# Performance work log

Measured on AMD Instinct MI355X. Metric: run time of the kernel, lower is better.

## Reference

```python
import jax, jax.numpy as jnp
import numpy as np
from jax import lax

# dims
B, N, D, H, K, NS = 16, 4096, 64, 128, 32, 1024  # clouds, pts/cloud, feat, hidden, max neighbors, fps samples
R = 0.2  # radius


def _fps(pos, n_s):
    """Farthest point sampling on one cloud. pos: [N,3] -> idx [n_s] int32."""
    n = pos.shape[0]

    def step(carry, _):
        dist, last = carry
        d = jnp.sum((pos - pos[last]) ** 2, axis=-1)
        dist = jnp.minimum(dist, d)
        nxt = jnp.argmax(dist).astype(jnp.int32)
        return (dist, nxt), last

    init = (jnp.full((n,), 1e10, pos.dtype), jnp.int32(0))
    _, idx = lax.scan(step, init, None, length=n_s)
    return idx


def setup_inputs() -> dict:
    key = jax.random.key(0)
    ks = jax.random.split(key, 6)
    s1 = 1.0 / np.sqrt(D + 1)
    s2 = 1.0 / np.sqrt(H)
    s3 = 1.0 / np.sqrt(D + H)
    return {
        "x": jax.random.normal(ks[0], (B, N, D), jnp.float32),
        "pos": jax.random.uniform(ks[1], (B, N, 3), jnp.float32),
        "W1": jax.random.normal(ks[2], (D + 1, H), jnp.float32) * s1,
        "b1": jnp.zeros((H,), jnp.float32),
        "W2": jax.random.normal(ks[3], (H, 3), jnp.float32) * s2,
        "b2": jnp.zeros((3,), jnp.float32),
        "W3": jax.random.normal(ks[4], (D + H, H), jnp.float32) * s3,
        "b3": jnp.zeros((H,), jnp.float32),
    }


def reference(x, pos, W1, b1, W2, b2, W3, b3):
    # 1) FPS downsample per cloud -> centers
    idx = jax.vmap(lambda p: _fps(p, NS))(pos)                    # [B,NS]
    pos_s = jax.vmap(lambda p, i: p[i])(pos, idx)                 # [B,NS,3]

    # 2) radius neighbor search: nearest-K within R (<= max_num_neighbors=32)
    d2 = jnp.sum((pos_s[:, :, None, :] - pos[:, None, :, :]) ** 2, axis=-1)  # [B,NS,N]
    masked = jnp.where(d2 <= R * R, d2, jnp.inf)
    neg, nbr = lax.top_k(-masked, K)                              # nearest K
    valid = (-neg) <= R * R                                       # [B,NS,K]

    # 3) gather neighbor features/positions
    x_j = jax.vmap(lambda a, i: a[i])(x, nbr)                     # [B,NS,K,D]
    pos_j = jax.vmap(lambda a, i: a[i])(pos, nbr)                 # [B,NS,K,3]
    diff = pos_j - pos_s[:, :, None, :]                           # pos_j - pos_i
    d2sel = jnp.sum(diff ** 2, axis=-1)
    dist = jnp.where(d2sel > 0, jnp.sqrt(jnp.where(d2sel > 0, d2sel, 1.0)), 0.0)

    # 4) message MLPs
    feat = jnp.concatenate([x_j, dist[..., None]], axis=-1)       # [B,NS,K,D+1]
    emb = jax.nn.relu(feat @ W1 + b1)                             # nn_msg_x
    pw = emb @ W2 + b2                                            # nn_msg_pos
    pmsg = diff * pw

    # 5) masked aggregate: sum for x, mean for pos
    m = valid[..., None].astype(emb.dtype)
    aggr_x = jnp.sum(emb * m, axis=2)                             # [B,NS,H]
    cnt = jnp.maximum(jnp.sum(m, axis=2), 1.0)                    # [B,NS,1]
    aggr_pos = jnp.sum(pmsg * m, axis=2) / cnt                    # [B,NS,3]

    # 6) update
    x_d = jax.vmap(lambda a, i: a[i])(x, idx)                     # [B,NS,D]
    out_x = jax.nn.relu(jnp.concatenate([x_d, aggr_x], axis=-1) @ W3 + b3)
    out_pos = pos_s + aggr_pos
    return out_x, out_pos, idx
```

## Files before the change

### kernel.cpp

```cpp
#include <hip/hip_runtime.h>
#include <math.h>

#define B_ 16
#define N_ 4096
#define D_ 64
#define H_ 128
#define K_ 32
#define NS_ 1024
#define R2_ 0.04f
#define CAP_ 1024

typedef short short8 __attribute__((ext_vector_type(8)));
typedef float f32x4 __attribute__((ext_vector_type(4)));
typedef unsigned short ushort_t;

static __device__ __forceinline__ short f2bf(float f) {
    unsigned u = __float_as_uint(f);
    unsigned r = (u + 0x7FFFu + ((u >> 16) & 1u)) >> 16;
    return (short)r;
}

template<int CTRL, int RM>
static __device__ __forceinline__ unsigned dppmov(unsigned v) {
    return (unsigned)__builtin_amdgcn_update_dpp((int)v, (int)v, CTRL, RM, 0xF, false);
}

#define DPP_FMAX_STEP(CTRL, RM)                                           \
    {                                                                     \
        float n = __uint_as_float(dppmov<CTRL, RM>(__float_as_uint(wm))); \
        wm = fmaxf(wm, n);                                                \
    }

#define DPP_UMIN_STEP(CTRL, RM)                                           \
    {                                                                     \
        unsigned n = dppmov<CTRL, RM>(cand);                              \
        cand = n < cand ? n : cand;                                       \
    }

#define DPP_UMIN_STEP_V(var, CTRL, RM)                                    \
    {                                                                     \
        unsigned n = dppmov<CTRL, RM>(var);                               \
        var = n < var ? n : var;                                          \
    }

__global__ __launch_bounds__(256) void cvt_kernel(
    const float* __restrict__ x, ushort_t* __restrict__ xb)
{
    const size_t i = ((size_t)blockIdx.x * 256 + threadIdx.x) * 8;
    float4 a = *(const float4*)(x + i);
    float4 c = *(const float4*)(x + i + 4);
    short8 o;
    o[0] = f2bf(a.x); o[1] = f2bf(a.y); o[2] = f2bf(a.z); o[3] = f2bf(a.w);
    o[4] = f2bf(c.x); o[5] = f2bf(c.y); o[6] = f2bf(c.z); o[7] = f2bf(c.w);
    *(short8*)(xb + i) = o;
}

__global__ __launch_bounds__(256, 1) void fps_kernel(
    const float* __restrict__ pos, int* __restrict__ idx_i,
    float* __restrict__ idx_f, float* __restrict__ pos_s)
{
    __shared__ float4 lpos4[N_];
    __shared__ float4 sres[NS_];
    __shared__ unsigned long long skey[2][4];
    __shared__ float4 scoord[2][4];
    const int b = blockIdx.x;
    const int t = threadIdx.x;
    const int wv = t >> 6;
    const int lane = t & 63;
    const float* posb = pos + (size_t)b * N_ * 3;
    for (int p = t; p < N_; p += 256)
        lpos4[p] = make_float4(posb[3 * p + 0], posb[3 * p + 1], posb[3 * p + 2], 0.f);
    __syncthreads();

    float px[16], py[16], pz[16], dist[16];
#pragma unroll
    for (int j = 0; j < 16; ++j) {
        float4 v = lpos4[t + 256 * j];
        px[j] = v.x; py[j] = v.y; pz[j] = v.z;
        dist[j] = 1e10f;
    }
    unsigned curidx = 0;
    float4 c0 = lpos4[0];
    float ccx = c0.x, ccy = c0.y, ccz = c0.z;

    for (int ns = 0; ns < NS_; ++ns) {
        if (t == 0)
            sres[ns] = make_float4(ccx, ccy, ccz, __uint_as_float(curidx));
        float bv = -1.f; int bj = 0;
#pragma unroll
        for (int j = 0; j < 16; ++j) {
            float dx = __fsub_rn(px[j], ccx);
            float dy = __fsub_rn(py[j], ccy);
            float dz = __fsub_rn(pz[j], ccz);
            float d2 = __fadd_rn(__fadd_rn(__fmul_rn(dx, dx), __fmul_rn(dy, dy)), __fmul_rn(dz, dz));
            float dn = fminf(dist[j], d2);
            dist[j] = dn;
            bool g = dn > bv;
            bv = g ? dn : bv;
            bj = g ? j : bj;
        }
        float wm = bv;
        DPP_FMAX_STEP(0x111, 0xF)
        DPP_FMAX_STEP(0x112, 0xF)
        DPP_FMAX_STEP(0x114, 0xF)
        DPP_FMAX_STEP(0x118, 0xF)
        DPP_FMAX_STEP(0x142, 0xA)
        DPP_FMAX_STEP(0x143, 0xC)
        const float wavemax = __uint_as_float(
            (unsigned)__builtin_amdgcn_readlane((int)__float_as_uint(wm), 63));
        const unsigned pidx = (unsigned)t + ((unsigned)bj << 8);
        const unsigned long long mask = __ballot(bv == wavemax);
        unsigned widx;
        if (__popcll(mask) == 1) {
            const int wl = __ffsll((long long)mask) - 1;
            widx = (unsigned)__builtin_amdgcn_readlane((int)pidx, wl);
        } else {
            unsigned cand = (bv == wavemax) ? pidx : 0xFFFFFFFFu;
            DPP_UMIN_STEP(0x111, 0xF)
            DPP_UMIN_STEP(0x112, 0xF)
            DPP_UMIN_STEP(0x114, 0xF)
            DPP_UMIN_STEP(0x118, 0xF)
            DPP_UMIN_STEP(0x142, 0xA)
            DPP_UMIN_STEP(0x143, 0xC)
            widx = (unsigned)__builtin_amdgcn_readlane((int)cand, 63);
        }
        float4 wc = lpos4[widx];
        if (lane == 0) {
            skey[ns & 1][wv] = (((unsigned long long)__float_as_uint(wavemax)) << 32)
                             | (unsigned long long)(0xFFFFFFFFu - widx);
            scoord[ns & 1][wv] = wc;
        }
        __syncthreads();
        {
            unsigned sid = (unsigned)(lane & 3);
            unsigned long long skv = skey[ns & 1][sid];
            float4 scv = scoord[ns & 1][sid];
            unsigned kh2 = (unsigned)(skv >> 32), kl2 = (unsigned)skv;
#define SLOT_STEP(CTRL)                                                        \
            {                                                                  \
                unsigned nh = dppmov<CTRL, 0xF>(kh2);                          \
                unsigned nl = dppmov<CTRL, 0xF>(kl2);                          \
                unsigned nsid = dppmov<CTRL, 0xF>(sid);                        \
                unsigned long long nk = (((unsigned long long)nh) << 32) | nl; \
                unsigned long long ok = (((unsigned long long)kh2) << 32) | kl2;\
                if (nk > ok) { kh2 = nh; kl2 = nl; sid = nsid; }               \
            }
            SLOT_STEP(0x101)
            SLOT_STEP(0x102)
#undef SLOT_STEP
            const int slotwin = __builtin_amdgcn_readfirstlane((int)sid);
            curidx = 0xFFFFFFFFu - (unsigned)__builtin_amdgcn_readfirstlane((int)kl2);
            ccx = __uint_as_float((unsigned)__builtin_amdgcn_readlane(
                      (int)__float_as_uint(scv.x), slotwin));
            ccy = __uint_as_float((unsigned)__builtin_amdgcn_readlane(
                      (int)__float_as_uint(scv.y), slotwin));
            ccz = __uint_as_float((unsigned)__builtin_amdgcn_readlane(
                      (int)__float_as_uint(scv.z), slotwin));
        }
    }
    __syncthreads();
    for (int i = t; i < NS_; i += 256) {
        float4 r = sres[i];
        unsigned id = __float_as_uint(r.w);
        idx_i[b * NS_ + i] = (int)id;
        idx_f[b * NS_ + i] = (float)id;
        pos_s[(b * NS_ + i) * 3 + 0] = r.x;
        pos_s[(b * NS_ + i) * 3 + 1] = r.y;
        pos_s[(b * NS_ + i) * 3 + 2] = r.z;
    }
}

__global__ __launch_bounds__(256) void nbr_kernel(
    const float* __restrict__ pos, const float* __restrict__ pos_s,
    int* __restrict__ nbr, float* __restrict__ cntv)
{
    __shared__ unsigned long long ck[4][CAP_];
    const int w = threadIdx.x >> 6;
    const int lane = threadIdx.x & 63;
    const int s = blockIdx.x * 4 + w;
    const int b = s >> 10;
    const float cx = pos_s[s * 3 + 0], cy = pos_s[s * 3 + 1], cz = pos_s[s * 3 + 2];
    const float* posb = pos + (size_t)b * N_ * 3;
    int m = 0;
    for (int base = 0; base < N_; base += 64) {
        int p = base + lane;
        float dx = __fsub_rn(posb[3 * p + 0], cx);
        float dy = __fsub_rn(posb[3 * p + 1], cy);
        float dz = __fsub_rn(posb[3 * p + 2], cz);
        float d2 = __fadd_rn(__fadd_rn(__fmul_rn(dx, dx), __fmul_rn(dy, dy)), __fmul_rn(dz, dz));
        bool in = (d2 <= R2_);
        unsigned long long msk = __ballot(in);
        int before = __popcll(msk & ((1ull << lane) - 1ull));
        int slot = m + before;
        if (in && slot < CAP_)
            ck[w][slot] = ((unsigned long long)__float_as_uint(d2) << 32) | (unsigned)p;
        m += __popcll(msk);
    }
    if (m > CAP_) m = CAP_;
    __asm__ volatile("s_waitcnt lgkmcnt(0)" ::: "memory");
    int kcnt = m < K_ ? m : K_;
    if (m <= 256) {
        unsigned long long kr[4];
#pragma unroll
        for (int r = 0; r < 4; ++r) {
            int q = r * 64 + lane;
            unsigned long long v = ck[w][q & (CAP_ - 1)];
            kr[r] = (q < m) ? v : ~0ull;
        }
        unsigned chosen = 0;
        for (int k = 0; k < kcnt; ++k) {
            unsigned long long localk = ~0ull; int br = -1;
#pragma unroll
            for (int r = 0; r < 4; ++r) {
                bool ok = (!((chosen >> r) & 1u)) && (kr[r] < localk);
                localk = ok ? kr[r] : localk;
                br = ok ? r : br;
            }
            const unsigned mybits = (unsigned)(localk >> 32);
            const unsigned myidx = (unsigned)localk;
            unsigned wb = mybits;
            DPP_UMIN_STEP_V(wb, 0x111, 0xF)
            DPP_UMIN_STEP_V(wb, 0x112, 0xF)
            DPP_UMIN_STEP_V(wb, 0x114, 0xF)
            DPP_UMIN_STEP_V(wb, 0x118, 0xF)
            DPP_UMIN_STEP_V(wb, 0x142, 0xA)
            DPP_UMIN_STEP_V(wb, 0x143, 0xC)
            const unsigned minbits = (unsigned)__builtin_amdgcn_readlane((int)wb, 63);
            const unsigned long long wmask = __ballot(mybits == minbits);
            unsigned widx;
            if (__popcll(wmask) == 1) {
                const int wl = __ffsll((long long)wmask) - 1;
                widx = (unsigned)__builtin_amdgcn_readlane((int)myidx, wl);
            } else {
                unsigned cand = (mybits == minbits) ? myidx : 0xFFFFFFFFu;
                DPP_UMIN_STEP(0x111, 0xF)
                DPP_UMIN_STEP(0x112, 0xF)
                DPP_UMIN_STEP(0x114, 0xF)
                DPP_UMIN_STEP(0x118, 0xF)
                DPP_UMIN_STEP(0x142, 0xA)
                DPP_UMIN_STEP(0x143, 0xC)
                widx = (unsigned)__builtin_amdgcn_readlane((int)cand, 63);
            }
            if (mybits == minbits && myidx == widx) chosen |= 1u << br;
            if (lane == 0) nbr[s * K_ + k] = (int)widx;
        }
    } else {
        unsigned chosen = 0;
        for (int k = 0; k < kcnt; ++k) {
            unsigned long long localk = ~0ull; int bslot = -1;
            for (int r = 0; r * 64 + lane < m; ++r) {
                if (chosen & (1u << r)) continue;
                int q = r * 64 + lane;
                unsigned long long key = ck[w][q];
                if (key < localk) { localk = key; bslot = q; }
            }
            unsigned kh = (unsigned)(localk >> 32), kl = (unsigned)localk;
#define DPP_MIN_STEP2(CTRL, RM)                                           \
            {                                                             \
                unsigned nh = dppmov<CTRL, RM>(kh);                       \
                unsigned nl = dppmov<CTRL, RM>(kl);                       \
                unsigned long long nk = (((unsigned long long)nh) << 32) | nl; \
                unsigned long long ok = (((unsigned long long)kh) << 32) | kl; \
                if (nk < ok) { kh = nh; kl = nl; }                        \
            }
            DPP_MIN_STEP2(0x111, 0xF)
            DPP_MIN_STEP2(0x112, 0xF)
            DPP_MIN_STEP2(0x114, 0xF)
            DPP_MIN_STEP2(0x118, 0xF)
            DPP_MIN_STEP2(0x142, 0xA)
            DPP_MIN_STEP2(0x143, 0xC)
#undef DPP_MIN_STEP2
            unsigned mh = (unsigned)__builtin_amdgcn_readlane((int)kh, 63);
            unsigned ml = (unsigned)__builtin_amdgcn_readlane((int)kl, 63);
            unsigned long long bk = (((unsigned long long)mh) << 32) | ml;
            if (localk == bk && bslot >= 0) chosen |= 1u << (bslot >> 6);
            if (lane == 0) nbr[s * K_ + k] = (int)(bk & 0xFFFFFFFFull);
        }
    }
    if (lane == 0) {
        for (int k = kcnt; k < K_; ++k) nbr[s * K_ + k] = -1;
        cntv[s] = (float)kcnt;
    }
}

__global__ __launch_bounds__(256) void msg_kernel(
    const ushort_t* __restrict__ xb, const float* __restrict__ pos,
    const float* __restrict__ W1, const float* __restrict__ b1,
    const float* __restrict__ W2, const float* __restrict__ b2,
    const float* __restrict__ pos_s, const int* __restrict__ nbr,
    const float* __restrict__ cntv, float* __restrict__ aggr_x,
    float* __restrict__ out_pos)
{
    __shared__ __align__(16) char smem[4 * 5120];
    const int t = threadIdx.x;
    const int wv = t >> 6, lane = t & 63;
    const int quad = lane >> 4, cl = lane & 15;
    char* wb = smem + wv * 5120;

    short8 bfrag[8][2];
    float b1v[8], w1dv[8], w2v0[8], w2v1[8], w2v2[8];
#pragma unroll
    for (int Nt = 0; Nt < 8; ++Nt) {
        const int h = Nt * 16 + cl;
#pragma unroll
        for (int ks = 0; ks < 2; ++ks) {
            short8 f;
#pragma unroll
            for (int jj = 0; jj < 8; ++jj)
                f[jj] = f2bf(W1[(ks * 32 + quad * 8 + jj) * H_ + h]);
            bfrag[Nt][ks] = f;
        }
        b1v[Nt] = b1[h];
        w1dv[Nt] = W1[64 * H_ + h];
        w2v0[Nt] = W2[h * 3 + 0];
        w2v1[Nt] = W2[h * 3 + 1];
        w2v2[Nt] = W2[h * 3 + 2];
    }
    const float b20 = b2[0], b21 = b2[1], b22 = b2[2];

    const int kkg = lane >> 1, half = lane & 1;
    for (int i = 0; i < 4; ++i) {
        const int s = blockIdx.x * 16 + wv * 4 + i;
        const int b = s >> 10;
        const int n = nbr[s * K_ + kkg];
        {
            char* frow = wb + kkg * 144 + half * 64;
            if (n >= 0) {
                const short8* xr = (const short8*)(xb + ((size_t)b * N_ + n) * D_) + half * 4;
#pragma unroll
                for (int q = 0; q < 4; ++q) *(short8*)(frow + q * 16) = xr[q];
            } else {
                short8 z = {0, 0, 0, 0, 0, 0, 0, 0};
#pragma unroll
                for (int q = 0; q < 4; ++q) *(short8*)(frow + q * 16) = z;
            }
            if (half == 0) {
                float dxm = 0.f, dym = 0.f, dzm = 0.f, de = -1.f;
                if (n >= 0) {
                    const float* pj = pos + ((size_t)b * N_ + n) * 3;
                    float dx = pj[0] - pos_s[s * 3 + 0];
                    float dy = pj[1] - pos_s[s * 3 + 1];
                    float dz = pj[2] - pos_s[s * 3 + 2];
                    float d2 = dx * dx + dy * dy + dz * dz;
                    de = d2 > 0.f ? sqrtf(d2) : 0.f;
                    dxm = dx; dym = dy; dzm = dz;
                }
                f32x4 sv = {dxm, dym, dzm, de};
                *(f32x4*)(wb + 4608 + kkg * 16) = sv;
            }
        }
        float agp[8] = {0, 0, 0, 0, 0, 0, 0, 0};
        float gp0[8] = {0, 0, 0, 0, 0, 0, 0, 0};
        float gp1[8] = {0, 0, 0, 0, 0, 0, 0, 0};
        float gp2[8] = {0, 0, 0, 0, 0, 0, 0, 0};
#pragma unroll
        for (int Mt = 0; Mt < 2; ++Mt) {
            short8 a0 = *(short8*)(wb + (Mt * 16 + cl) * 144 + quad * 16);
            short8 a1 = *(short8*)(wb + (Mt * 16 + cl) * 144 + 64 + quad * 16);
            f32x4 acc[8];
#pragma unroll
            for (int Nt = 0; Nt < 8; ++Nt) {
                f32x4 z = {0.f, 0.f, 0.f, 0.f};
                z = __builtin_amdgcn_mfma_f32_16x16x32_bf16(a0, bfrag[Nt][0], z, 0, 0, 0);
                z = __builtin_amdgcn_mfma_f32_16x16x32_bf16(a1, bfrag[Nt][1], z, 0, 0, 0);
                acc[Nt] = z;
            }
            f32x4 sd[4];
#pragma unroll
            for (int r = 0; r < 4; ++r)
                sd[r] = *(f32x4*)(wb + 4608 + (Mt * 16 + quad * 4 + r) * 16);
#pragma unroll
            for (int Nt = 0; Nt < 8; ++Nt) {
#pragma unroll
                for (int r = 0; r < 4; ++r) {
                    float dr = sd[r][3];
                    float wgt = dr >= 0.f ? 1.f : 0.f;
                    float dd = dr >= 0.f ? dr : 0.f;
                    float e = fmaf(dd, w1dv[Nt], acc[Nt][r]) + b1v[Nt];
                    e = e > 0.f ? e : 0.f;
                    agp[Nt] = fmaf(wgt, e, agp[Nt]);
                    gp0[Nt] = fmaf(sd[r][0], e, gp0[Nt]);
                    gp1[Nt] = fmaf(sd[r][1], e, gp1[Nt]);
                    gp2[Nt] = fmaf(sd[r][2], e, gp2[Nt]);
                }
            }
        }
#pragma unroll
        for (int Nt = 0; Nt < 8; ++Nt) {
            float v = agp[Nt]; v += __shfl_xor(v, 16); v += __shfl_xor(v, 32);
            aggr_x[(size_t)s * H_ + Nt * 16 + cl] = v;
            float g0 = gp0[Nt]; g0 += __shfl_xor(g0, 16); g0 += __shfl_xor(g0, 32); gp0[Nt] = g0;
            float g1 = gp1[Nt]; g1 += __shfl_xor(g1, 16); g1 += __shfl_xor(g1, 32); gp1[Nt] = g1;
            float g2 = gp2[Nt]; g2 += __shfl_xor(g2, 16); g2 += __shfl_xor(g2, 32); gp2[Nt] = g2;
        }
        float pr0 = 0.f, pr1 = 0.f, pr2 = 0.f;
#pragma unroll
        for (int Nt = 0; Nt < 8; ++Nt) {
            pr0 = fmaf(w2v0[Nt], gp0[Nt], pr0);
            pr1 = fmaf(w2v1[Nt], gp1[Nt], pr1);
            pr2 = fmaf(w2v2[Nt], gp2[Nt], pr2);
        }
#pragma unroll
        for (int off = 1; off < 16; off <<= 1) {
            pr0 += __shfl_xor(pr0, off);
            pr1 += __shfl_xor(pr1, off);
            pr2 += __shfl_xor(pr2, off);
        }
        f32x4 dsv = *(f32x4*)(wb + 4608 + (lane & 31) * 16);
        float q0 = dsv[0], q1 = dsv[1], q2 = dsv[2];
#pragma unroll
        for (int off = 1; off < 32; off <<= 1) {
            q0 += __shfl_xor(q0, off);
            q1 += __shfl_xor(q1, off);
            q2 += __shfl_xor(q2, off);
        }
        float cnt = cntv[s]; if (cnt < 1.f) cnt = 1.f;
        if (lane < 3) {
            float pr = lane == 0 ? pr0 : (lane == 1 ? pr1 : pr2);
            float qq = lane == 0 ? q0 : (lane == 1 ? q1 : q2);
            float bb = lane == 0 ? b20 : (lane == 1 ? b21 : b22);
            out_pos[s * 3 + lane] = pos_s[s * 3 + lane] + (pr + bb * qq) / cnt;
        }
    }
}

__global__ __launch_bounds__(128) void out_kernel(
    const float* __restrict__ x, const float* __restrict__ W3,
    const float* __restrict__ b3, const int* __restrict__ idx_i,
    const float* __restrict__ aggr_x, float* __restrict__ out_x)
{
    __shared__ float rows[32][208];
    const int t = threadIdx.x;
    const int s0 = blockIdx.x * 32;
    const int sl = t >> 2, part = t & 3;
    const int s = s0 + sl;
    const int b = s >> 10;
    const int id = idx_i[s];
    {
        const float4* xr = (const float4*)(x + ((size_t)b * N_ + id) * D_);
        float4* rr = (float4*)&rows[sl][0];
#pragma unroll
        for (int q = 0; q < 4; ++q) rr[part * 4 + q] = xr[part * 4 + q];
        const float4* ar = (const float4*)(aggr_x + (size_t)s * H_);
        float4* rr2 = (float4*)&rows[sl][64];
#pragma unroll
        for (int q = 0; q < 8; ++q) rr2[part * 8 + q] = ar[part * 8 + q];
    }
    __syncthreads();
    float acc[32];
#pragma unroll
    for (int i = 0; i < 32; ++i) acc[i] = 0.f;
    for (int j4 = 0; j4 < 48; ++j4) {
        float w0 = W3[(j4 * 4 + 0) * H_ + t];
        float w1 = W3[(j4 * 4 + 1) * H_ + t];
        float w2 = W3[(j4 * 4 + 2) * H_ + t];
        float w3 = W3[(j4 * 4 + 3) * H_ + t];
#pragma unroll
        for (int i = 0; i < 32; ++i) {
            const float4 f = *(const float4*)&rows[i][j4 * 4];
            float a = acc[i];
            a = fmaf(f.x, w0, a); a = fmaf(f.y, w1, a);
            a = fmaf(f.z, w2, a); a = fmaf(f.w, w3, a);
            acc[i] = a;
        }
    }
    const float bb = b3[t];
#pragma unroll
    for (int i = 0; i < 32; ++i) {
        float v = acc[i] + bb;
        v = v > 0.f ? v : 0.f;
        out_x[(size_t)(s0 + i) * H_ + t] = v;
    }
}

extern "C" void kernel_launch(void* const* d_in, const int* in_sizes, int n_in,
                              void* d_out, int out_size, void* d_ws, size_t ws_size,
                              hipStream_t stream) {
    const float* x   = (const float*)d_in[0];
    const float* pos = (const float*)d_in[1];
    const float* W1  = (const float*)d_in[2];
    const float* b1  = (const float*)d_in[3];
    const float* W2  = (const float*)d_in[4];
    const float* b2  = (const float*)d_in[5];
    const float* W3  = (const float*)d_in[6];
    const float* b3  = (const float*)d_in[7];

    float* out_x   = (float*)d_out;
    float* out_pos = (float*)d_out + 2097152;
    float* idx_f   = (float*)d_out + 2146304;

    char* ws = (char*)d_ws;
    int*      idx_i  = (int*)ws;
    float*    pos_s  = (float*)(ws + 65536);
    int*      nbr    = (int*)(ws + 262144);
    float*    cntv   = (float*)(ws + 2359296);
    float*    aggr_x = (float*)(ws + 2424832);
    ushort_t* x_bf16 = (ushort_t*)(ws + 10813440);

    cvt_kernel<<<(B_ * N_ * D_) / (256 * 8), 256, 0, stream>>>(x, x_bf16);
    fps_kernel<<<B_, 256, 0, stream>>>(pos, idx_i, idx_f, pos_s);
    nbr_kernel<<<(B_ * NS_) / 4, 256, 0, stream>>>(pos, pos_s, nbr, cntv);
    msg_kernel<<<(B_ * NS_) / 16, 256, 0, stream>>>(x_bf16, pos, W1, b1, W2, b2,
                                                    pos_s, nbr, cntv, aggr_x, out_pos);
    out_kernel<<<(B_ * NS_) / 32, 128, 0, stream>>>(x, W3, b3, idx_i, aggr_x, out_x);
}
```

Measured before the change: 968.3 us.

## Merge bf16 conversion into FPS launch and pack FPS distance math

The separate x-to-bf16 conversion kernel is folded into the FPS launch as extra blocks, so the conversion runs on otherwise idle CUs alongside the 16 serial FPS blocks and one launch disappears. The FPS inner loop now uses packed v_pk_add/v_pk_mul on pairs of points, which halves the VALU instructions for the distance computation. The per-thread argmax is rebuilt as a tree reduction instead of a serial chain, shortening the dependency chain on the serial critical path. One risk is that the FPS blocks must actually be scheduled first, otherwise conversion blocks could delay them. Another is that rounding order has to match the reference argmax exactly.

After: 1.179 ms. 1.22x slower.

```diff
diff --git a/kernel.cpp b/kernel.cpp
--- a/kernel.cpp
+++ b/kernel.cpp
@@ -12,6 +12,7 @@
 
 typedef short short8 __attribute__((ext_vector_type(8)));
 typedef float f32x4 __attribute__((ext_vector_type(4)));
+typedef float f32x2 __attribute__((ext_vector_type(2)));
 typedef unsigned short ushort_t;
 
 static __device__ __forceinline__ short f2bf(float f) {
@@ -20,6 +21,17 @@
     return (short)r;
 }
 
+static __device__ __forceinline__ f32x2 pk_add(f32x2 a, f32x2 b) {
+    f32x2 d;
+    asm("v_pk_add_f32 %0, %1, %2" : "=v"(d) : "v"(a), "v"(b));
+    return d;
+}
+static __device__ __forceinline__ f32x2 pk_mul(f32x2 a, f32x2 b) {
+    f32x2 d;
+    asm("v_pk_mul_f32 %0, %1, %2" : "=v"(d) : "v"(a), "v"(b));
+    return d;
+}
+
 template<int CTRL, int RM>
 static __device__ __forceinline__ unsigned dppmov(unsigned v) {
     return (unsigned)__builtin_amdgcn_update_dpp((int)v, (int)v, CTRL, RM, 0xF, false);
@@ -43,28 +55,28 @@
         var = n < var ? n : var;                                          \
     }
 
-__global__ __launch_bounds__(256) void cvt_kernel(
-    const float* __restrict__ x, ushort_t* __restrict__ xb)
-{
-    const size_t i = ((size_t)blockIdx.x * 256 + threadIdx.x) * 8;
-    float4 a = *(const float4*)(x + i);
-    float4 c = *(const float4*)(x + i + 4);
-    short8 o;
-    o[0] = f2bf(a.x); o[1] = f2bf(a.y); o[2] = f2bf(a.z); o[3] = f2bf(a.w);
-    o[4] = f2bf(c.x); o[5] = f2bf(c.y); o[6] = f2bf(c.z); o[7] = f2bf(c.w);
-    *(short8*)(xb + i) = o;
-}
-
 __global__ __launch_bounds__(256, 1) void fps_kernel(
     const float* __restrict__ pos, int* __restrict__ idx_i,
-    float* __restrict__ idx_f, float* __restrict__ pos_s)
+    float* __restrict__ idx_f, float* __restrict__ pos_s,
+    const float* __restrict__ x, ushort_t* __restrict__ xb)
 {
     __shared__ float4 lpos4[N_];
     __shared__ float4 sres[NS_];
     __shared__ unsigned long long skey[2][4];
     __shared__ float4 scoord[2][4];
-    const int b = blockIdx.x;
+    const int bid = blockIdx.x;
     const int t = threadIdx.x;
+    if (bid >= B_) {
+        const size_t i = ((size_t)(bid - B_) * 256 + t) * 8;
+        float4 a = *(const float4*)(x + i);
+        float4 c = *(const float4*)(x + i + 4);
+        short8 o;
+        o[0] = f2bf(a.x); o[1] = f2bf(a.y); o[2] = f2bf(a.z); o[3] = f2bf(a.w);
+        o[4] = f2bf(c.x); o[5] = f2bf(c.y); o[6] = f2bf(c.z); o[7] = f2bf(c.w);
+        *(short8*)(xb + i) = o;
+        return;
+    }
+    const int b = bid;
     const int wv = t >> 6;
     const int lane = t & 63;
     const float* posb = pos + (size_t)b * N_ * 3;
@@ -72,12 +84,15 @@
         lpos4[p] = make_float4(posb[3 * p + 0], posb[3 * p + 1], posb[3 * p + 2], 0.f);
     __syncthreads();
 
-    float px[16], py[16], pz[16], dist[16];
-#pragma unroll
-    for (int j = 0; j < 16; ++j) {
-        float4 v = lpos4[t + 256 * j];
-        px[j] = v.x; py[j] = v.y; pz[j] = v.z;
-        dist[j] = 1e10f;
+    f32x2 px[8], py[8], pz[8], dist[8];
+#pragma unroll
+    for (int q = 0; q < 8; ++q) {
+        float4 v0 = lpos4[t + 256 * (2 * q)];
+        float4 v1 = lpos4[t + 256 * (2 * q + 1)];
+        px[q].x = v0.x; px[q].y = v1.x;
+        py[q].x = v0.y; py[q].y = v1.y;
+        pz[q].x = v0.z; pz[q].y = v1.z;
+        dist[q].x = 1e10f; dist[q].y = 1e10f;
     }
     unsigned curidx = 0;
     float4 c0 = lpos4[0];
@@ -86,19 +101,49 @@
     for (int ns = 0; ns < NS_; ++ns) {
         if (t == 0)
             sres[ns] = make_float4(ccx, ccy, ccz, __uint_as_float(curidx));
-        float bv = -1.f; int bj = 0;
-#pragma unroll
-        for (int j = 0; j < 16; ++j) {
-            float dx = __fsub_rn(px[j], ccx);
-            float dy = __fsub_rn(py[j], ccy);
-            float dz = __fsub_rn(pz[j], ccz);
-            float d2 = __fadd_rn(__fadd_rn(__fmul_rn(dx, dx), __fmul_rn(dy, dy)), __fmul_rn(dz, dz));
-            float dn = fminf(dist[j], d2);
-            dist[j] = dn;
-            bool g = dn > bv;
-            bv = g ? dn : bv;
-            bj = g ? j : bj;
-        }
+        const float nx = -ccx, ny = -ccy, nz = -ccz;
+        f32x2 cxn; cxn.x = nx; cxn.y = nx;
+        f32x2 cyn; cyn.x = ny; cyn.y = ny;
+        f32x2 czn; czn.x = nz; czn.y = nz;
+        float dn[16];
+#pragma unroll
+        for (int q = 0; q < 8; ++q) {
+            f32x2 dx = pk_add(px[q], cxn);
+            f32x2 dy = pk_add(py[q], cyn);
+            f32x2 dz = pk_add(pz[q], czn);
+            f32x2 xx = pk_mul(dx, dx);
+            f32x2 yy = pk_mul(dy, dy);
+            f32x2 ss = pk_add(xx, yy);
+            f32x2 zz = pk_mul(dz, dz);
+            f32x2 d2 = pk_add(ss, zz);
+            float a = fminf(dist[q].x, d2.x);
+            float c = fminf(dist[q].y, d2.y);
+            dist[q].x = a; dist[q].y = c;
+            dn[2 * q] = a; dn[2 * q + 1] = c;
+        }
+        float va[8]; int ja[8];
+#pragma unroll
+        for (int q = 0; q < 8; ++q) {
+            bool g = dn[2 * q + 1] > dn[2 * q];
+            va[q] = g ? dn[2 * q + 1] : dn[2 * q];
+            ja[q] = g ? 2 * q + 1 : 2 * q;
+        }
+#pragma unroll
+        for (int q = 0; q < 4; ++q) {
+            bool g = va[2 * q + 1] > va[2 * q];
+            va[q] = g ? va[2 * q + 1] : va[2 * q];
+            ja[q] = g ? ja[2 * q + 1] : ja[2 * q];
+        }
+        {
+            bool g1 = va[1] > va[0];
+            float u0 = g1 ? va[1] : va[0]; int i0 = g1 ? ja[1] : ja[0];
+            bool g2 = va[3] > va[2];
+            float u1 = g2 ? va[3] : va[2]; int i1 = g2 ? ja[3] : ja[2];
+            bool g3 = u1 > u0;
+            va[0] = g3 ? u1 : u0; ja[0] = g3 ? i1 : i0;
+        }
+        const float bv = va[0];
+        const int bj = ja[0];
         float wm = bv;
         DPP_FMAX_STEP(0x111, 0xF)
         DPP_FMAX_STEP(0x112, 0xF)
@@ -497,8 +542,8 @@
     float*    aggr_x = (float*)(ws + 2424832);
     ushort_t* x_bf16 = (ushort_t*)(ws + 10813440);
 
-    cvt_kernel<<<(B_ * N_ * D_) / (256 * 8), 256, 0, stream>>>(x, x_bf16);
-    fps_kernel<<<B_, 256, 0, stream>>>(pos, idx_i, idx_f, pos_s);
+    const int cvt_blocks = (B_ * N_ * D_) / (256 * 8);
+    fps_kernel<<<B_ + cvt_blocks, 256, 0, stream>>>(pos, idx_i, idx_f, pos_s, x, x_bf16);
     nbr_kernel<<<(B_ * NS_) / 4, 256, 0, stream>>>(pos, pos_s, nbr, cntv);
     msg_kernel<<<(B_ * NS_) / 16, 256, 0, stream>>>(x_bf16, pos, W1, b1, W2, b2,
                                                     pos_s, nbr, cntv, aggr_x, out_pos);
```
